# Optimization experiments

Measured on AMD Instinct MI355X. Metric: run time of the kernel, lower is better.

## Reference

```python
import math
import jax, jax.numpy as jnp
import numpy as np

N = 2048
HID = 1024
ALPHA = 0.5
BETA = 0.1  # greedy term is zero when coords is None


def setup_inputs() -> dict:
    key = jax.random.key(0)
    k1, k2, k3, k4 = jax.random.split(key, 4)
    node_emb = jax.random.normal(k1, (N, HID), jnp.float32)
    demands = jax.random.uniform(k2, (N,), jnp.float32)  # each < 1 << capacity
    # query_net: Linear(hid+2 -> hid); key_net: Linear(hid -> hid)
    Wq = jax.random.normal(k3, (HID, HID + 2), jnp.float32) / math.sqrt(HID + 2)
    bq = jnp.zeros((HID,), jnp.float32)
    Wk = jax.random.normal(k4, (HID, HID), jnp.float32) / math.sqrt(HID)
    bk = jnp.zeros((HID,), jnp.float32)
    return {"node_emb": node_emb, "demands": demands, "Wq": Wq, "bq": bq,
            "Wk": Wk, "bk": bk, "capacity": 40, "depot_idx": 0}


def _decode(node_emb, demands, Wq, bq, Wk, bk, capacity, depot_idx):
    n, h = node_emb.shape
    cap = jnp.float32(capacity)
    inv_sqrt = 1.0 / math.sqrt(h)
    # key_net is a per-node linear map: precompute once (same math as per-step gather+linear)
    K = node_emb @ Wk.T + bk  # [N, H]
    idx = jnp.arange(n)
    # demands < 1, capacity = 40 => >= 39 customers per route => few depot returns;
    # T = N + N//8 safely bounds customer picks + route-closing depot emissions.
    T = n + n // 8
    visited0 = jnp.zeros((n,), bool).at[depot_idx].set(True)

    def step(carry, _):
        visited, load, last, done = carry
        feasible = (~visited) & (demands <= load)
        has_cand = jnp.any(feasible)
        # context = [emb(last), load/capacity, avgd]; avgd = 0 since coords is None
        ctx = jnp.concatenate([node_emb[last],
                               jnp.stack([load / cap, jnp.float32(0.0)])])
        q = Wq @ ctx + bq                      # [H]
        s = ALPHA * ((K @ q) * inv_sqrt)       # [N] scores over all nodes
        s_m = jnp.where(feasible, s, -jnp.inf)
        cand = jnp.argmax(s_m)
        take = has_cand & (~done)
        nxt = jnp.where(take, cand, depot_idx).astype(jnp.int32)
        step_score = jnp.where(take, s[cand], jnp.float32(0.0))
        visited = visited | ((idx == cand) & take)
        load = jnp.where(take, load - demands[cand], cap)  # route end resets load
        done = done | ((~take) & jnp.all(visited))
        return (visited, load, nxt, done), (nxt, step_score)

    carry0 = (visited0, cap, jnp.int32(depot_idx), jnp.bool_(False))
    _, (seq, scores) = jax.lax.scan(step, carry0, None, length=T)
    tour = jnp.concatenate([jnp.array([depot_idx], seq.dtype), seq])  # [T+1]
    return tour, scores


def reference(node_emb, demands, Wq, bq, Wk, bk, capacity, depot_idx):
    # tour: flat visitation order; routes are the segments between depot occurrences
    # (trailing depots are padding once all customers are served).
    # scores: selected decoder score at each step (0 at depot/padding steps).
    return _decode(node_emb, demands, Wq, bq, Wk, bk, capacity, depot_idx)
```

## Files before the change

kernel.cpp:

```cpp
#include <hip/hip_runtime.h>
#include <hip/hip_bf16.h>


#define NN 2048
#define HH 1024
#define TSTEPS (NN + NN / 8)
#define TILE 64
#define KT 16
#define KCAND 128

__global__ __launch_bounds__(256) void prep_wqh(const float* __restrict__ Wq,
                                                float* __restrict__ Wqh) {
  int id = blockIdx.x * 256 + threadIdx.x;
  int r = id >> 10, c = id & 1023;
  Wqh[id] = Wq[r * (HH + 2) + c];
}

__global__ __launch_bounds__(256) void gemm_nt(const float* __restrict__ A, int lda,
                                               const float* __restrict__ B, int ldb,
                                               float* __restrict__ C, int ldc,
                                               int K, const float* __restrict__ bias) {
  __shared__ float As[KT][TILE + 4];
  __shared__ float Bs[KT][TILE + 4];
  const int i0 = blockIdx.y * TILE;
  const int j0 = blockIdx.x * TILE;
  const int t = threadIdx.x;
  const int srow = t >> 2, sq = t & 3;
  const int tx = t & 15, ty = t >> 4;
  float acc[4][4] = {};
  for (int k0 = 0; k0 < K; k0 += KT) {
    float4 av = *(const float4*)&A[(size_t)(i0 + srow) * lda + k0 + sq * 4];
    float4 bv = *(const float4*)&B[(size_t)(j0 + srow) * ldb + k0 + sq * 4];
    __syncthreads();
    As[sq * 4 + 0][srow] = av.x; As[sq * 4 + 1][srow] = av.y;
    As[sq * 4 + 2][srow] = av.z; As[sq * 4 + 3][srow] = av.w;
    Bs[sq * 4 + 0][srow] = bv.x; Bs[sq * 4 + 1][srow] = bv.y;
    Bs[sq * 4 + 2][srow] = bv.z; Bs[sq * 4 + 3][srow] = bv.w;
    __syncthreads();
#pragma unroll
    for (int k = 0; k < KT; ++k) {
      float4 a4 = *(const float4*)&As[k][ty * 4];
      float4 b4 = *(const float4*)&Bs[k][tx * 4];
      float a[4] = {a4.x, a4.y, a4.z, a4.w};
      float b[4] = {b4.x, b4.y, b4.z, b4.w};
#pragma unroll
      for (int m = 0; m < 4; ++m)
#pragma unroll
        for (int n = 0; n < 4; ++n) acc[m][n] = fmaf(a[m], b[n], acc[m][n]);
    }
  }
  float bb[4] = {0.f, 0.f, 0.f, 0.f};
  if (bias) {
#pragma unroll
    for (int n = 0; n < 4; ++n) bb[n] = bias[j0 + tx * 4 + n];
  }
#pragma unroll
  for (int m = 0; m < 4; ++m) {
    float4 st = {acc[m][0] + bb[0], acc[m][1] + bb[1], acc[m][2] + bb[2], acc[m][3] + bb[3]};
    *(float4*)&C[(size_t)(i0 + ty * 4 + m) * ldc + j0 + tx * 4] = st;
  }
}

__global__ __launch_bounds__(64) void uv_k(const float* __restrict__ Kmat,
                                           const float* __restrict__ Wq,
                                           const float* __restrict__ bq,
                                           float* __restrict__ u, float* __restrict__ v) {
  int i = blockIdx.x;
  int lane = threadIdx.x;
  float su = 0.f, sv = 0.f;
#pragma unroll
  for (int m = 0; m < HH / 64; ++m) {
    int j = lane + 64 * m;
    float kv = Kmat[(size_t)i * HH + j];
    su = fmaf(kv, Wq[(size_t)j * (HH + 2) + HH], su);
    sv = fmaf(kv, bq[j], sv);
  }
#pragma unroll
  for (int off = 32; off; off >>= 1) {
    su += __shfl_down(su, off, 64);
    sv += __shfl_down(sv, off, 64);
  }
  if (lane == 0) { u[i] = su; v[i] = sv; }
}

__global__ __launch_bounds__(256) void umax_k(const float* __restrict__ u,
                                              float* __restrict__ umaxp) {
  __shared__ float sm[256];
  int t = threadIdx.x;
  float m = 0.f;
  for (int i = t; i < NN; i += 256) m = fmaxf(m, fabsf(u[i]));
  sm[t] = m;
  __syncthreads();
  for (int s = 128; s; s >>= 1) {
    if (t < s) sm[t] = fmaxf(sm[t], sm[t + s]);
    __syncthreads();
  }
  if (t == 0) *umaxp = sm[0];
}

__device__ __forceinline__ unsigned f2key(float f) {
  unsigned x = __float_as_uint(f);
  return x ^ ((x >> 31) ? 0xFFFFFFFFu : 0x80000000u);
}
__device__ __forceinline__ float key2f(unsigned k) {
  unsigned x = (k & 0x80000000u) ? (k ^ 0x80000000u) : ~k;
  return __uint_as_float(x);
}
__global__ __launch_bounds__(256) void prep_cand(const float* __restrict__ GT,
                                                 uint2* __restrict__ cand,
                                                 float* __restrict__ thr) {
  __shared__ float rowv[NN];
  __shared__ int hist[256];
  __shared__ int s_d, s_need, s_gt, s_eq;
  const int row = blockIdx.x, t = threadIdx.x;
  for (int i = t; i < NN; i += 256) rowv[i] = GT[(size_t)row * NN + i];
  __syncthreads();
  unsigned prefix = 0;
  int need = KCAND;
  for (int pass = 0; pass < 4; ++pass) {
    hist[t] = 0;
    __syncthreads();
    const int shift = 24 - 8 * pass;
    for (int i = t; i < NN; i += 256) {
      unsigned k = f2key(rowv[i]);
      if (pass == 0 || (k >> (shift + 8)) == (prefix >> (shift + 8)))
        atomicAdd(&hist[(k >> shift) & 0xFF], 1);
    }
    __syncthreads();
    if (t == 0) {
      int cum = 0, d = 255;
      for (; d > 0; --d) {
        if (cum + hist[d] >= need) break;
        cum += hist[d];
      }
      s_d = d;
      s_need = need - cum;
    }
    __syncthreads();
    prefix |= ((unsigned)s_d) << shift;
    need = s_need;
    __syncthreads();
  }
  const unsigned thrk = prefix;
  if (t == 0) { s_gt = 0; s_eq = 0; thr[row] = key2f(thrk); }
  __syncthreads();
  for (int i = t; i < NN; i += 256) {
    if (f2key(rowv[i]) > thrk) {
      int p = atomicAdd(&s_gt, 1);
      cand[(size_t)row * KCAND + p] = make_uint2(__float_as_uint(rowv[i]), (unsigned)i);
    }
  }
  __syncthreads();
  const int cgt = s_gt;
  for (int i = t; i < NN; i += 256) {
    if (f2key(rowv[i]) == thrk) {
      int p = atomicAdd(&s_eq, 1);
      if (p < KCAND - cgt)
        cand[(size_t)row * KCAND + cgt + p] = make_uint2(__float_as_uint(rowv[i]), (unsigned)i);
    }
  }
}

__global__ __launch_bounds__(256) void warm_k(const float* __restrict__ a, int n,
                                              const float* __restrict__ b, int m,
                                              float* __restrict__ sink) {
  float s = 0.f;
  const float4* a4 = (const float4*)a;
  for (int i = threadIdx.x; i < n / 4; i += 256) {
    float4 x = a4[i];
    s += x.x + x.y + x.z + x.w;
  }
  for (int i = threadIdx.x; i < m; i += 256) s += b[i];
  if (s == 1.2345e-30f) sink[blockIdx.x] = s;
}

#define DPP_MERGE2(CTRL)                                                      \
  {                                                                           \
    int ovb = __builtin_amdgcn_update_dpp(                                    \
        (int)0xFF800000, __float_as_int(bv), (CTRL), 0xf, 0xf, false);        \
    int oib = __builtin_amdgcn_update_dpp(                                    \
        0x7fffffff, bi, (CTRL), 0xf, 0xf, false);                             \
    float ov = __int_as_float(ovb);                                           \
    if (ov > bv || (ov == bv && oib < bi)) { bv = ov; bi = oib; }             \
  }

__global__ __launch_bounds__(64, 1) void decode(const float* __restrict__ GT,
                                                const uint2* __restrict__ cand,
                                                const float* __restrict__ thrp,
                                                const float* __restrict__ umaxp,
                                                const float* __restrict__ u,
                                                const float* __restrict__ demands,
                                                const int* __restrict__ capp,
                                                const int* __restrict__ depotp,
                                                float* __restrict__ out) {
  __shared__ __align__(16) float s_dem[NN];
  __shared__ __align__(16) float s_dd[NN];
  __shared__ __align__(16) float s_u[NN];
  __shared__ __align__(16) uint4 s_dcand[KCAND / 2];
  __shared__ __align__(16) float s_tour[TSTEPS + 1];
  __shared__ __align__(16) float s_lr[TSTEPS];

  const int lane = threadIdx.x;
  const int depot = *depotp;
  const float capf = (float)(*capp);
  const float umaxv = *umaxp;
  const float INF = __builtin_inff();
  const float NEGINF = -INF;
  const float C0 = 0.015625f;
  const float MARGIN = 0.5f;

  for (int i = lane; i < NN; i += 64) {
    float d = demands[i];
    s_dem[i] = d;
    s_dd[i] = d;
    s_u[i] = u[i];
  }
  const uint4* dc4 = (const uint4*)(cand + (size_t)depot * KCAND);
  for (int i = lane; i < KCAND / 2; i += 64) s_dcand[i] = dc4[i];
  const float thrd = thrp[depot];
  __syncthreads();
  if (lane == 0) {
    s_dd[depot] = INF;
    s_tour[0] = (float)depot;
  }

  float uu[32];
#pragma unroll
  for (int r = 0; r < 8; ++r) {
    float4 u4 = ((const float4*)u)[r * 64 + lane];
    uu[r * 4 + 0] = u4.x; uu[r * 4 + 1] = u4.y;
    uu[r * 4 + 2] = u4.z; uu[r * 4 + 3] = u4.w;
  }

  const float4* dd4 = (const float4*)s_dd;

  int done = 0, ntaken = 0, lasts = depot;
  float load = capf;
  float lr = load / capf;
  float thrcur = thrd;
  uint4 ca = dc4[lane];

  for (int step = 0; step < TSTEPS; ++step) {
    if (done) {
      const float df = (float)depot;
      for (int q = step + lane; q < TSTEPS; q += 64) {
        s_tour[1 + q] = df;
        s_lr[q] = -1.0f;
      }
      break;
    }
    float bv = NEGINF;
    int bi = 0x7fffffff;
    {
      float g0 = __uint_as_float(ca.x); int i0 = (int)ca.y;
      float g1 = __uint_as_float(ca.z); int i1 = (int)ca.w;
      float d0 = s_dd[i0], u0 = s_u[i0];
      float d1 = s_dd[i1], u1 = s_u[i1];
      float t0 = fmaf(u0, lr, g0);
      float t1 = fmaf(u1, lr, g1);
      if ((d0 <= load) && (t0 > bv || (t0 == bv && i0 < bi))) { bv = t0; bi = i0; }
      if ((d1 <= load) && (t1 > bv || (t1 == bv && i1 < bi))) { bv = t1; bi = i1; }
    }
    DPP_MERGE2(0x111); DPP_MERGE2(0x112); DPP_MERGE2(0x114);
    DPP_MERGE2(0x118); DPP_MERGE2(0x142); DPP_MERGE2(0x143);
    float rbv = __int_as_float(__builtin_amdgcn_readlane(__float_as_int(bv), 63));
    int rbi = __builtin_amdgcn_readlane(bi, 63);

    const float B = fmaf(lr, umaxv, thrcur) + MARGIN;
    int take, nxt;
    if (rbv > B) {
      take = 1; nxt = rbi;
    } else {
      const float4* rowp = (const float4*)(GT + (size_t)lasts * NN);
      float bv = NEGINF;
      int bi = NN;
#pragma unroll
      for (int r = 0; r < 8; ++r) {
        float4 g4 = rowp[r * 64 + lane];
        float4 d4 = dd4[r * 64 + lane];
        float gl[4] = {g4.x, g4.y, g4.z, g4.w};
        float dl[4] = {d4.x, d4.y, d4.z, d4.w};
        float cv = NEGINF;
        int cj = 0;
#pragma unroll
        for (int j = 0; j < 4; ++j) {
          float tt = fmaf(uu[r * 4 + j], lr, gl[j]);
          bool feas = (dl[j] <= load);
          if (feas && tt > cv) { cv = tt; cj = j; }
        }
        if (cv > bv) { bv = cv; bi = 4 * (r * 64 + lane) + cj; }
      }
      DPP_MERGE2(0x111); DPP_MERGE2(0x112); DPP_MERGE2(0x114);
      DPP_MERGE2(0x118); DPP_MERGE2(0x142); DPP_MERGE2(0x143);
      float fbv = __int_as_float(__builtin_amdgcn_readlane(__float_as_int(bv), 63));
      rbi = __builtin_amdgcn_readlane(bi, 63);
      take = (fbv > NEGINF);
      nxt = take ? rbi : depot;
    }

    if (nxt == depot) {
      ca = s_dcand[lane];
      thrcur = thrd;
    } else {
      const uint4* rc4 = (const uint4*)(cand + (size_t)nxt * KCAND);
      ca = rc4[lane];
      thrcur = thrp[nxt];
    }

    if (lane == 0) {
      s_tour[1 + step] = (float)nxt;
      s_lr[step] = take ? lr : -1.0f;
    }
    if (take) {
      load = load - s_dem[rbi];
      ntaken++;
      if (lane == 0) s_dd[rbi] = INF;
    } else {
      load = capf;
      if (ntaken == NN - 1) done = 1;
    }
    lasts = nxt;
    lr = load / capf;
  }

  for (int i = lane; i <= TSTEPS; i += 64) out[i] = s_tour[i];
  for (int s = lane; s < TSTEPS; s += 64) {
    float lrs = s_lr[s];
    float sc = 0.0f;
    if (lrs >= 0.0f) {
      int lastI = (int)s_tour[s];
      int biI = (int)s_tour[s + 1];
      float g = GT[(size_t)lastI * NN + biI];
      sc = fmaf(u[biI], lrs, g) * C0;
    }
    out[1 + TSTEPS + s] = sc;
  }
}

extern "C" void kernel_launch(void* const* d_in, const int* in_sizes, int n_in,
                              void* d_out, int out_size, void* d_ws, size_t ws_size,
                              hipStream_t stream) {
  const float* emb     = (const float*)d_in[0];
  const float* demands = (const float*)d_in[1];
  const float* Wq      = (const float*)d_in[2];
  const float* bq      = (const float*)d_in[3];
  const float* Wk      = (const float*)d_in[4];
  const float* bk      = (const float*)d_in[5];
  const int* cap       = (const int*)d_in[6];
  const int* depot     = (const int*)d_in[7];
  float* out           = (float*)d_out;

  char* ws = (char*)d_ws;
  float* Kmat = (float*)(ws);
  float* Z    = (float*)(ws + ((size_t)8 << 20));
  float* GT   = (float*)(ws + ((size_t)16 << 20));
  float* Wqh  = (float*)(ws + ((size_t)32 << 20));
  float* u    = (float*)(ws + ((size_t)36 << 20));
  float* v    = (float*)(ws + ((size_t)36 << 20) + 8192);
  float* thr  = (float*)(ws + ((size_t)36 << 20) + 16384);
  float* umax = (float*)(ws + ((size_t)36 << 20) + 24576);
  float* sink = (float*)(ws + ((size_t)36 << 20) + 32768);
  uint2* cnd  = (uint2*)Wqh;

  hipLaunchKernelGGL(prep_wqh, dim3(4096), dim3(256), 0, stream, Wq, Wqh);
  hipLaunchKernelGGL(gemm_nt, dim3(HH / TILE, NN / TILE), dim3(256), 0, stream,
                     emb, HH, Wk, HH, Kmat, HH, HH, bk);
  hipLaunchKernelGGL(gemm_nt, dim3(HH / TILE, NN / TILE), dim3(256), 0, stream,
                     emb, HH, Wqh, HH, Z, HH, HH, (const float*)nullptr);
  hipLaunchKernelGGL(uv_k, dim3(NN), dim3(64), 0, stream, Kmat, Wq, bq, u, v);
  hipLaunchKernelGGL(umax_k, dim3(1), dim3(256), 0, stream, u, umax);
  hipLaunchKernelGGL(gemm_nt, dim3(NN / TILE, NN / TILE), dim3(256), 0, stream,
                     Z, HH, Kmat, HH, GT, NN, HH, v);
  hipLaunchKernelGGL(prep_cand, dim3(NN), dim3(256), 0, stream, GT, cnd, thr);
  hipLaunchKernelGGL(warm_k, dim3(128), dim3(256), 0, stream,
                     (const float*)cnd, NN * KCAND * 2, thr, NN, sink);
  hipLaunchKernelGGL(decode, dim3(1), dim3(64), 0, stream, GT, cnd, thr, umax,
                     u, demands, cap, depot, out);
}
```

Before: 2.043 ms.

## Add compact top-15 packed candidate tier in LDS before 128-candidate fallback

prep_cand now also picks the top-15 candidates per row and packs each into one 32-bit word holding a truncated score key and an 11-bit index. It also writes a per-row threshold, set to infinity when scores are too large for the truncation to be safe. The decode kernel copies all packed lists into LDS and checks this first tier with a top-2 DPP reduction plus margin tests. It falls back to the 128-candidate global list and then to a full row scan only when needed. The step loop is unrolled by three with software-prefetched candidate loads, trading a large LDS footprint and extra prep work for shorter serial per-step latency.

Measured after the change: 2.202 ms. 7.8% more time.

```diff
diff --git a/kernel.cpp b/kernel.cpp
--- a/kernel.cpp
+++ b/kernel.cpp
@@ -8,6 +8,7 @@
 #define TILE 64
 #define KT 16
 #define KCAND 128
+#define KL 15
 
 __global__ __launch_bounds__(256) void prep_wqh(const float* __restrict__ Wq,
                                                 float* __restrict__ Wqh) {
@@ -108,10 +109,14 @@
 }
 __global__ __launch_bounds__(256) void prep_cand(const float* __restrict__ GT,
                                                  uint2* __restrict__ cand,
-                                                 float* __restrict__ thr) {
+                                                 float* __restrict__ thr,
+                                                 unsigned* __restrict__ pc16,
+                                                 float* __restrict__ thr16) {
   __shared__ float rowv[NN];
   __shared__ int hist[256];
-  __shared__ int s_d, s_need, s_gt, s_eq;
+  __shared__ unsigned c128k[KCAND];
+  __shared__ int c128i[KCAND];
+  __shared__ int s_d, s_need, s_gt, s_eq, s_gt2, s_eq2, s_flag;
   const int row = blockIdx.x, t = threadIdx.x;
   for (int i = t; i < NN; i += 256) rowv[i] = GT[(size_t)row * NN + i];
   __syncthreads();
@@ -145,9 +150,12 @@
   if (t == 0) { s_gt = 0; s_eq = 0; thr[row] = key2f(thrk); }
   __syncthreads();
   for (int i = t; i < NN; i += 256) {
-    if (f2key(rowv[i]) > thrk) {
+    unsigned k = f2key(rowv[i]);
+    if (k > thrk) {
       int p = atomicAdd(&s_gt, 1);
       cand[(size_t)row * KCAND + p] = make_uint2(__float_as_uint(rowv[i]), (unsigned)i);
+      c128k[p] = k;
+      c128i[p] = i;
     }
   }
   __syncthreads();
@@ -155,10 +163,62 @@
   for (int i = t; i < NN; i += 256) {
     if (f2key(rowv[i]) == thrk) {
       int p = atomicAdd(&s_eq, 1);
-      if (p < KCAND - cgt)
+      if (p < KCAND - cgt) {
         cand[(size_t)row * KCAND + cgt + p] = make_uint2(__float_as_uint(rowv[i]), (unsigned)i);
-    }
-  }
+        c128k[cgt + p] = thrk;
+        c128i[cgt + p] = i;
+      }
+    }
+  }
+  __syncthreads();
+  unsigned pfx2 = 0;
+  need = KL;
+  for (int pass = 0; pass < 4; ++pass) {
+    hist[t] = 0;
+    __syncthreads();
+    const int shift = 24 - 8 * pass;
+    for (int i = t; i < KCAND; i += 256) {
+      unsigned k = c128k[i];
+      if (pass == 0 || (k >> (shift + 8)) == (pfx2 >> (shift + 8)))
+        atomicAdd(&hist[(k >> shift) & 0xFF], 1);
+    }
+    __syncthreads();
+    if (t == 0) {
+      int cum = 0, d = 255;
+      for (; d > 0; --d) {
+        if (cum + hist[d] >= need) break;
+        cum += hist[d];
+      }
+      s_d = d;
+      s_need = need - cum;
+    }
+    __syncthreads();
+    pfx2 |= ((unsigned)s_d) << shift;
+    need = s_need;
+    __syncthreads();
+  }
+  const unsigned thrk15 = pfx2;
+  if (t == 0) { s_gt2 = 0; s_eq2 = 0; s_flag = 0; }
+  __syncthreads();
+  for (int i = t; i < KCAND; i += 256) {
+    if (c128k[i] > thrk15) {
+      int p = atomicAdd(&s_gt2, 1);
+      pc16[(size_t)row * KL + p] = (c128k[i] & 0xFFFFF800u) | (unsigned)c128i[i];
+      if (fabsf(key2f(c128k[i])) >= 128.0f) s_flag = 1;
+    }
+  }
+  __syncthreads();
+  const int cgt2 = s_gt2;
+  for (int i = t; i < KCAND; i += 256) {
+    if (c128k[i] == thrk15) {
+      int p = atomicAdd(&s_eq2, 1);
+      if (p < KL - cgt2)
+        pc16[(size_t)row * KL + cgt2 + p] = (thrk15 & 0xFFFFF800u) | (unsigned)c128i[i];
+    }
+  }
+  if (t == 0 && fabsf(key2f(thrk15)) >= 128.0f) s_flag = 1;
+  __syncthreads();
+  if (t == 0) thr16[row] = s_flag ? __builtin_inff() : key2f(thrk15);
 }
 
 __global__ __launch_bounds__(256) void warm_k(const float* __restrict__ a, int n,
@@ -184,21 +244,38 @@
     if (ov > bv || (ov == bv && oib < bi)) { bv = ov; bi = oib; }             \
   }
 
+#define DPP_TOP2(CTRL)                                                        \
+  {                                                                           \
+    int ovb = __builtin_amdgcn_update_dpp(                                    \
+        (int)0xFF800000, __float_as_int(bv1), (CTRL), 0xf, 0xf, false);       \
+    int oib = __builtin_amdgcn_update_dpp(                                    \
+        0x7fffffff, bi1, (CTRL), 0xf, 0xf, false);                            \
+    int ov2b = __builtin_amdgcn_update_dpp(                                   \
+        (int)0xFF800000, __float_as_int(bv2), (CTRL), 0xf, 0xf, false);       \
+    float ov1 = __int_as_float(ovb);                                          \
+    float ov2 = __int_as_float(ov2b);                                         \
+    float lose = fminf(bv1, ov1);                                             \
+    if (ov1 > bv1 || (ov1 == bv1 && oib < bi1)) { bv1 = ov1; bi1 = oib; }     \
+    bv2 = fmaxf(fmaxf(bv2, ov2), lose);                                       \
+  }
+
 __global__ __launch_bounds__(64, 1) void decode(const float* __restrict__ GT,
                                                 const uint2* __restrict__ cand,
                                                 const float* __restrict__ thrp,
+                                                const unsigned* __restrict__ pc16,
+                                                const float* __restrict__ thr16,
                                                 const float* __restrict__ umaxp,
                                                 const float* __restrict__ u,
                                                 const float* __restrict__ demands,
                                                 const int* __restrict__ capp,
                                                 const int* __restrict__ depotp,
                                                 float* __restrict__ out) {
-  __shared__ __align__(16) float s_dem[NN];
+  __shared__ __align__(16) unsigned s_pc[NN * KL + 64];
   __shared__ __align__(16) float s_dd[NN];
   __shared__ __align__(16) float s_u[NN];
-  __shared__ __align__(16) uint4 s_dcand[KCAND / 2];
-  __shared__ __align__(16) float s_tour[TSTEPS + 1];
+  __shared__ __align__(16) float s_thr[NN];
   __shared__ __align__(16) float s_lr[TSTEPS];
+  __shared__ __align__(16) unsigned short s_tour[TSTEPS + 2];
 
   const int lane = threadIdx.x;
   const int depot = *depotp;
@@ -208,122 +285,143 @@
   const float NEGINF = -INF;
   const float C0 = 0.015625f;
   const float MARGIN = 0.5f;
+  const float EGM = 0.0625f;
 
   for (int i = lane; i < NN; i += 64) {
-    float d = demands[i];
-    s_dem[i] = d;
-    s_dd[i] = d;
+    s_dd[i] = demands[i];
     s_u[i] = u[i];
-  }
-  const uint4* dc4 = (const uint4*)(cand + (size_t)depot * KCAND);
-  for (int i = lane; i < KCAND / 2; i += 64) s_dcand[i] = dc4[i];
-  const float thrd = thrp[depot];
-  __syncthreads();
+    s_thr[i] = thr16[i];
+  }
+  {
+    const uint4* p4 = (const uint4*)pc16;
+    uint4* q4 = (uint4*)s_pc;
+    for (int i = lane; i < NN * KL / 4; i += 64) q4[i] = p4[i];
+  }
   if (lane == 0) {
     s_dd[depot] = INF;
-    s_tour[0] = (float)depot;
-  }
-
-  float uu[32];
-#pragma unroll
-  for (int r = 0; r < 8; ++r) {
-    float4 u4 = ((const float4*)u)[r * 64 + lane];
-    uu[r * 4 + 0] = u4.x; uu[r * 4 + 1] = u4.y;
-    uu[r * 4 + 2] = u4.z; uu[r * 4 + 3] = u4.w;
-  }
-
-  const float4* dd4 = (const float4*)s_dd;
+    s_tour[0] = (unsigned short)depot;
+  }
 
   int done = 0, ntaken = 0, lasts = depot;
   float load = capf;
   float lr = load / capf;
-  float thrcur = thrd;
-  uint4 ca = dc4[lane];
-
-  for (int step = 0; step < TSTEPS; ++step) {
-    if (done) {
-      const float df = (float)depot;
-      for (int q = step + lane; q < TSTEPS; q += 64) {
-        s_tour[1 + q] = df;
-        s_lr[q] = -1.0f;
-      }
-      break;
-    }
-    float bv = NEGINF;
-    int bi = 0x7fffffff;
-    {
-      float g0 = __uint_as_float(ca.x); int i0 = (int)ca.y;
-      float g1 = __uint_as_float(ca.z); int i1 = (int)ca.w;
-      float d0 = s_dd[i0], u0 = s_u[i0];
-      float d1 = s_dd[i1], u1 = s_u[i1];
-      float t0 = fmaf(u0, lr, g0);
-      float t1 = fmaf(u1, lr, g1);
-      if ((d0 <= load) && (t0 > bv || (t0 == bv && i0 < bi))) { bv = t0; bi = i0; }
-      if ((d1 <= load) && (t1 > bv || (t1 == bv && i1 < bi))) { bv = t1; bi = i1; }
-    }
-    DPP_MERGE2(0x111); DPP_MERGE2(0x112); DPP_MERGE2(0x114);
-    DPP_MERGE2(0x118); DPP_MERGE2(0x142); DPP_MERGE2(0x143);
-    float rbv = __int_as_float(__builtin_amdgcn_readlane(__float_as_int(bv), 63));
-    int rbi = __builtin_amdgcn_readlane(bi, 63);
-
-    const float B = fmaf(lr, umaxv, thrcur) + MARGIN;
-    int take, nxt;
-    if (rbv > B) {
-      take = 1; nxt = rbi;
-    } else {
-      const float4* rowp = (const float4*)(GT + (size_t)lasts * NN);
-      float bv = NEGINF;
-      int bi = NN;
-#pragma unroll
-      for (int r = 0; r < 8; ++r) {
-        float4 g4 = rowp[r * 64 + lane];
-        float4 d4 = dd4[r * 64 + lane];
-        float gl[4] = {g4.x, g4.y, g4.z, g4.w};
-        float dl[4] = {d4.x, d4.y, d4.z, d4.w};
-        float cv = NEGINF;
-        int cj = 0;
-#pragma unroll
-        for (int j = 0; j < 4; ++j) {
-          float tt = fmaf(uu[r * 4 + j], lr, gl[j]);
-          bool feas = (dl[j] <= load);
-          if (feas && tt > cv) { cv = tt; cj = j; }
-        }
-        if (cv > bv) { bv = cv; bi = 4 * (r * 64 + lane) + cj; }
-      }
-      DPP_MERGE2(0x111); DPP_MERGE2(0x112); DPP_MERGE2(0x114);
-      DPP_MERGE2(0x118); DPP_MERGE2(0x142); DPP_MERGE2(0x143);
-      float fbv = __int_as_float(__builtin_amdgcn_readlane(__float_as_int(bv), 63));
-      rbi = __builtin_amdgcn_readlane(bi, 63);
-      take = (fbv > NEGINF);
-      nxt = take ? rbi : depot;
-    }
-
-    if (nxt == depot) {
-      ca = s_dcand[lane];
-      thrcur = thrd;
-    } else {
-      const uint4* rc4 = (const uint4*)(cand + (size_t)nxt * KCAND);
-      ca = rc4[lane];
-      thrcur = thrp[nxt];
-    }
-
-    if (lane == 0) {
-      s_tour[1 + step] = (float)nxt;
-      s_lr[step] = take ? lr : -1.0f;
-    }
-    if (take) {
-      load = load - s_dem[rbi];
-      ntaken++;
-      if (lane == 0) s_dd[rbi] = INF;
-    } else {
-      load = capf;
-      if (ntaken == NN - 1) done = 1;
-    }
-    lasts = nxt;
-    lr = load / capf;
-  }
-
-  for (int i = lane; i <= TSTEPS; i += 64) out[i] = s_tour[i];
+  int step = 0;
+  uint4 cc0, cc1, cc2;
+  float th0, th1, th2;
+
+#define STEP_ONE(CC, TH)                                                        \
+  {                                                                             \
+    if (done) goto FLUSH;                                                       \
+    const int row = lasts;                                                      \
+                          \
+    CC = ((const uint4*)(cand + (size_t)row * KCAND))[lane];                    \
+    TH = thrp[row];                                                             \
+                                \
+    unsigned pw = s_pc[row * KL + lane];                                        \
+    float thr1 = s_thr[row];                                                    \
+    int i1x = (int)(pw & 0x7FFu);                                               \
+    float g1 = key2f(pw & 0xFFFFF800u);         \
+    float d1 = s_dd[i1x];                                                       \
+    float su1 = s_u[i1x];                                                       \
+    float t1 = fmaf(su1, lr, g1);                                               \
+    bool act = (lane < KL) && (d1 <= load);                                     \
+    float bv1 = act ? t1 : NEGINF;                                              \
+    int bi1 = act ? i1x : 0x7fffffff;                                           \
+    float bv2 = NEGINF;                                                         \
+    DPP_TOP2(0x111); DPP_TOP2(0x112); DPP_TOP2(0x114);                          \
+    DPP_TOP2(0x118); DPP_TOP2(0x142); DPP_TOP2(0x143);                          \
+    float rv1 = __int_as_float(__builtin_amdgcn_readlane(__float_as_int(bv1), 63)); \
+    int ri1 = __builtin_amdgcn_readlane(bi1, 63);                               \
+    float rv2 = __int_as_float(__builtin_amdgcn_readlane(__float_as_int(bv2), 63)); \
+    const float B1 = fmaf(lr, umaxv, thr1) + MARGIN;                            \
+    int take, nxt;                                                              \
+    if (rv1 > B1 && rv1 > rv2 + EGM) {                                          \
+            \
+      take = 1; nxt = ri1;                                                      \
+    } else {                                                                    \
+           \
+      float bv = NEGINF;                                                        \
+      int bi = 0x7fffffff;                                                      \
+      {                                                                         \
+        float ga = __uint_as_float(CC.x); int ia = (int)CC.y;                   \
+        float gb = __uint_as_float(CC.z); int ib = (int)CC.w;                   \
+        float da = s_dd[ia], ua = s_u[ia];                                      \
+        float db = s_dd[ib], ub = s_u[ib];                                      \
+        float ta = fmaf(ua, lr, ga);                                            \
+        float tb = fmaf(ub, lr, gb);                                            \
+        if ((da <= load) && (ta > bv || (ta == bv && ia < bi))) { bv = ta; bi = ia; } \
+        if ((db <= load) && (tb > bv || (tb == bv && ib < bi))) { bv = tb; bi = ib; } \
+      }                                                                         \
+      DPP_MERGE2(0x111); DPP_MERGE2(0x112); DPP_MERGE2(0x114);                  \
+      DPP_MERGE2(0x118); DPP_MERGE2(0x142); DPP_MERGE2(0x143);                  \
+      float rbv = __int_as_float(__builtin_amdgcn_readlane(__float_as_int(bv), 63)); \
+      int rbi = __builtin_amdgcn_readlane(bi, 63);                              \
+      const float B2 = fmaf(lr, umaxv, TH) + MARGIN;                            \
+      if (rbv > B2) {                                                           \
+        take = 1; nxt = rbi;                                                    \
+      } else {                                                                  \
+                              \
+        const float4* rowp = (const float4*)(GT + (size_t)row * NN);            \
+        const float4* dd4 = (const float4*)s_dd;                                \
+        const float4* uu4 = (const float4*)s_u;                                 \
+        float fv = NEGINF;                                                      \
+        int fi = NN;                                                            \
+        _Pragma("unroll") for (int r = 0; r < 8; ++r) {                         \
+          float4 g4 = rowp[r * 64 + lane];                                      \
+          float4 d4v = dd4[r * 64 + lane];                                      \
+          float4 u4v = uu4[r * 64 + lane];                                      \
+          float gl[4] = {g4.x, g4.y, g4.z, g4.w};                               \
+          float dl[4] = {d4v.x, d4v.y, d4v.z, d4v.w};                           \
+          float ul[4] = {u4v.x, u4v.y, u4v.z, u4v.w};                           \
+          float cv = NEGINF;                                                    \
+          int cj = 0;                                                           \
+          _Pragma("unroll") for (int j = 0; j < 4; ++j) {                       \
+            float tt = fmaf(ul[j], lr, gl[j]);                                  \
+            bool feas = (dl[j] <= load);                                        \
+            if (feas && tt > cv) { cv = tt; cj = j; }                           \
+          }                                                                     \
+          if (cv > fv) { fv = cv; fi = 4 * (r * 64 + lane) + cj; }              \
+        }                                                                       \
+        float bv = fv;                                                          \
+        int bi = fi;                                                            \
+        DPP_MERGE2(0x111); DPP_MERGE2(0x112); DPP_MERGE2(0x114);                \
+        DPP_MERGE2(0x118); DPP_MERGE2(0x142); DPP_MERGE2(0x143);                \
+        float fbv = __int_as_float(__builtin_amdgcn_readlane(__float_as_int(bv), 63)); \
+        int fbi = __builtin_amdgcn_readlane(bi, 63);                            \
+        take = (fbv > NEGINF) ? 1 : 0;                                          \
+        nxt = take ? fbi : depot;                                               \
+      }                                                                         \
+    }                                                                           \
+        \
+    if (lane == 0) {                                                            \
+      s_tour[1 + step] = (unsigned short)nxt;                                   \
+      s_lr[step] = take ? lr : -1.0f;                                           \
+    }                                                                           \
+    if (take) {                                                                 \
+      float dwin = s_dd[nxt];          \
+      load = load - dwin;                                                       \
+      ntaken++;                                                                 \
+      if (lane == 0) s_dd[nxt] = INF;                                           \
+    } else {                                                                    \
+      load = capf;                                                              \
+      if (ntaken == NN - 1) done = 1;                                           \
+    }                                                                           \
+    lasts = nxt;                                                                \
+    lr = load / capf;                                                           \
+    ++step;                                                                     \
+  }
+
+  for (int s3 = 0; s3 < TSTEPS; s3 += 3) {
+    STEP_ONE(cc0, th0)
+    STEP_ONE(cc1, th1)
+    STEP_ONE(cc2, th2)
+  }
+FLUSH:
+  for (int q = step + lane; q < TSTEPS; q += 64) {
+    s_tour[1 + q] = (unsigned short)depot;
+    s_lr[q] = -1.0f;
+  }
+  for (int i = lane; i <= TSTEPS; i += 64) out[i] = (float)s_tour[i];
   for (int s = lane; s < TSTEPS; s += 64) {
     float lrs = s_lr[s];
     float sc = 0.0f;
@@ -331,10 +429,11 @@
       int lastI = (int)s_tour[s];
       int biI = (int)s_tour[s + 1];
       float g = GT[(size_t)lastI * NN + biI];
-      sc = fmaf(u[biI], lrs, g) * C0;
+      sc = fmaf(s_u[biI], lrs, g) * C0;
     }
     out[1 + TSTEPS + s] = sc;
   }
+#undef STEP_ONE
 }
 
 extern "C" void kernel_launch(void* const* d_in, const int* in_sizes, int n_in,
@@ -361,6 +460,8 @@
   float* umax = (float*)(ws + ((size_t)36 << 20) + 24576);
   float* sink = (float*)(ws + ((size_t)36 << 20) + 32768);
   uint2* cnd  = (uint2*)Wqh;
+  unsigned* pc16g = (unsigned*)(ws + ((size_t)34 << 20));
+  float* thr16g   = (float*)(ws + ((size_t)34 << 20) + (128 << 10));
 
   hipLaunchKernelGGL(prep_wqh, dim3(4096), dim3(256), 0, stream, Wq, Wqh);
   hipLaunchKernelGGL(gemm_nt, dim3(HH / TILE, NN / TILE), dim3(256), 0, stream,
@@ -371,9 +472,10 @@
   hipLaunchKernelGGL(umax_k, dim3(1), dim3(256), 0, stream, u, umax);
   hipLaunchKernelGGL(gemm_nt, dim3(NN / TILE, NN / TILE), dim3(256), 0, stream,
                      Z, HH, Kmat, HH, GT, NN, HH, v);
-  hipLaunchKernelGGL(prep_cand, dim3(NN), dim3(256), 0, stream, GT, cnd, thr);
+  hipLaunchKernelGGL(prep_cand, dim3(NN), dim3(256), 0, stream, GT, cnd, thr,
+                     pc16g, thr16g);
   hipLaunchKernelGGL(warm_k, dim3(128), dim3(256), 0, stream,
                      (const float*)cnd, NN * KCAND * 2, thr, NN, sink);
-  hipLaunchKernelGGL(decode, dim3(1), dim3(64), 0, stream, GT, cnd, thr, umax,
-                     u, demands, cap, depot, out);
-}
+  hipLaunchKernelGGL(decode, dim3(1), dim3(64), 0, stream, GT, cnd, thr,
+                     pc16g, thr16g, umax, u, demands, cap, depot, out);
+}
```

## Add packed top-15 candidate tier in LDS ahead of top-128 fallback

Applied to the files above, without the earlier changes.

Prep now also extracts each row's top-15 candidates, packed as truncated score bits plus an 11-bit index, and stores two bf16-rounded thresholds per row. The decode kernel keeps the whole top-15 table in LDS and picks from it using a top-2 DPP reduction with a gap check. It falls back to the global top-128 list and then to the full GT row only when that pick is not certifiably correct. This removes most per-step global memory loads from the serial decode loop, but costs a heavier prep pass, about 120KB of LDS, and relies on quantised scores being exact enough to keep argmax results correct.

New measurement: 1.905 ms. -6.8%, faster.

```diff
diff --git a/kernel.cpp b/kernel.cpp
--- a/kernel.cpp
+++ b/kernel.cpp
@@ -8,6 +8,7 @@
 #define TILE 64
 #define KT 16
 #define KCAND 128
+#define KL 15
 
 __global__ __launch_bounds__(256) void prep_wqh(const float* __restrict__ Wq,
                                                 float* __restrict__ Wqh) {
@@ -106,12 +107,20 @@
   unsigned x = (k & 0x80000000u) ? (k ^ 0x80000000u) : ~k;
   return __uint_as_float(x);
 }
+__device__ __forceinline__ unsigned ub16(float x) {
+  unsigned b = __float_as_uint(x);
+  if (x > 0.f && (b & 0xFFFFu)) b += 0x10000u;
+  return b >> 16;
+}
 __global__ __launch_bounds__(256) void prep_cand(const float* __restrict__ GT,
                                                  uint2* __restrict__ cand,
-                                                 float* __restrict__ thr) {
+                                                 unsigned* __restrict__ pc16,
+                                                 unsigned* __restrict__ thrpk) {
   __shared__ float rowv[NN];
   __shared__ int hist[256];
-  __shared__ int s_d, s_need, s_gt, s_eq;
+  __shared__ unsigned c128k[KCAND];
+  __shared__ int c128i[KCAND];
+  __shared__ int s_d, s_need, s_gt, s_eq, s_gt2, s_eq2, s_flag;
   const int row = blockIdx.x, t = threadIdx.x;
   for (int i = t; i < NN; i += 256) rowv[i] = GT[(size_t)row * NN + i];
   __syncthreads();
@@ -142,12 +151,15 @@
     __syncthreads();
   }
   const unsigned thrk = prefix;
-  if (t == 0) { s_gt = 0; s_eq = 0; thr[row] = key2f(thrk); }
+  if (t == 0) { s_gt = 0; s_eq = 0; }
   __syncthreads();
   for (int i = t; i < NN; i += 256) {
-    if (f2key(rowv[i]) > thrk) {
+    unsigned k = f2key(rowv[i]);
+    if (k > thrk) {
       int p = atomicAdd(&s_gt, 1);
       cand[(size_t)row * KCAND + p] = make_uint2(__float_as_uint(rowv[i]), (unsigned)i);
+      c128k[p] = k;
+      c128i[p] = i;
     }
   }
   __syncthreads();
@@ -155,14 +167,68 @@
   for (int i = t; i < NN; i += 256) {
     if (f2key(rowv[i]) == thrk) {
       int p = atomicAdd(&s_eq, 1);
-      if (p < KCAND - cgt)
+      if (p < KCAND - cgt) {
         cand[(size_t)row * KCAND + cgt + p] = make_uint2(__float_as_uint(rowv[i]), (unsigned)i);
-    }
+        c128k[cgt + p] = thrk;
+        c128i[cgt + p] = i;
+      }
+    }
+  }
+  __syncthreads();
+  unsigned pfx2 = 0;
+  need = KL;
+  for (int pass = 0; pass < 4; ++pass) {
+    hist[t] = 0;
+    __syncthreads();
+    const int shift = 24 - 8 * pass;
+    for (int i = t; i < KCAND; i += 256) {
+      unsigned k = c128k[i];
+      if (pass == 0 || (k >> (shift + 8)) == (pfx2 >> (shift + 8)))
+        atomicAdd(&hist[(k >> shift) & 0xFF], 1);
+    }
+    __syncthreads();
+    if (t == 0) {
+      int cum = 0, d = 255;
+      for (; d > 0; --d) {
+        if (cum + hist[d] >= need) break;
+        cum += hist[d];
+      }
+      s_d = d;
+      s_need = need - cum;
+    }
+    __syncthreads();
+    pfx2 |= ((unsigned)s_d) << shift;
+    need = s_need;
+    __syncthreads();
+  }
+  const unsigned thrk15 = pfx2;
+  if (t == 0) { s_gt2 = 0; s_eq2 = 0; s_flag = 0; }
+  __syncthreads();
+  for (int i = t; i < KCAND; i += 256) {
+    if (c128k[i] > thrk15) {
+      int p = atomicAdd(&s_gt2, 1);
+      pc16[(size_t)row * KL + p] = (c128k[i] & 0xFFFFF800u) | (unsigned)c128i[i];
+      if (fabsf(key2f(c128k[i])) >= 128.0f) s_flag = 1;
+    }
+  }
+  __syncthreads();
+  const int cgt2 = s_gt2;
+  for (int i = t; i < KCAND; i += 256) {
+    if (c128k[i] == thrk15) {
+      int p = atomicAdd(&s_eq2, 1);
+      if (p < KL - cgt2)
+        pc16[(size_t)row * KL + cgt2 + p] = (thrk15 & 0xFFFFF800u) | (unsigned)c128i[i];
+    }
+  }
+  if (t == 0 && fabsf(key2f(thrk15)) >= 128.0f) s_flag = 1;
+  __syncthreads();
+  if (t == 0) {
+    float t15 = s_flag ? __builtin_inff() : key2f(thrk15);
+    thrpk[row] = (ub16(t15) << 16) | ub16(key2f(thrk));
   }
 }
 
 __global__ __launch_bounds__(256) void warm_k(const float* __restrict__ a, int n,
-                                              const float* __restrict__ b, int m,
                                               float* __restrict__ sink) {
   float s = 0.f;
   const float4* a4 = (const float4*)a;
@@ -170,7 +236,6 @@
     float4 x = a4[i];
     s += x.x + x.y + x.z + x.w;
   }
-  for (int i = threadIdx.x; i < m; i += 256) s += b[i];
   if (s == 1.2345e-30f) sink[blockIdx.x] = s;
 }
 
@@ -184,21 +249,36 @@
     if (ov > bv || (ov == bv && oib < bi)) { bv = ov; bi = oib; }             \
   }
 
+#define DPP_TOP2(CTRL)                                                        \
+  {                                                                           \
+    int ovb = __builtin_amdgcn_update_dpp(                                    \
+        (int)0xFF800000, __float_as_int(bv1), (CTRL), 0xf, 0xf, false);       \
+    int oib = __builtin_amdgcn_update_dpp(                                    \
+        0x7fffffff, bi1, (CTRL), 0xf, 0xf, false);                            \
+    int ov2b = __builtin_amdgcn_update_dpp(                                   \
+        (int)0xFF800000, __float_as_int(bv2), (CTRL), 0xf, 0xf, false);       \
+    float ov1 = __int_as_float(ovb);                                          \
+    float ov2 = __int_as_float(ov2b);                                         \
+    float lose = fminf(bv1, ov1);                                             \
+    if (ov1 > bv1 || (ov1 == bv1 && oib < bi1)) { bv1 = ov1; bi1 = oib; }     \
+    bv2 = fmaxf(fmaxf(bv2, ov2), lose);                                       \
+  }
+
 __global__ __launch_bounds__(64, 1) void decode(const float* __restrict__ GT,
                                                 const uint2* __restrict__ cand,
-                                                const float* __restrict__ thrp,
+                                                const unsigned* __restrict__ pc16,
+                                                const unsigned* __restrict__ thrpkg,
                                                 const float* __restrict__ umaxp,
                                                 const float* __restrict__ u,
                                                 const float* __restrict__ demands,
                                                 const int* __restrict__ capp,
                                                 const int* __restrict__ depotp,
                                                 float* __restrict__ out) {
-  __shared__ __align__(16) float s_dem[NN];
-  __shared__ __align__(16) float s_dd[NN];
-  __shared__ __align__(16) float s_u[NN];
-  __shared__ __align__(16) uint4 s_dcand[KCAND / 2];
-  __shared__ __align__(16) float s_tour[TSTEPS + 1];
+  __shared__ __align__(16) unsigned s_pc[NN * KL + 64];
+  __shared__ __align__(16) float2 s_du[NN];
+  __shared__ __align__(16) unsigned s_thr[NN];
   __shared__ __align__(16) float s_lr[TSTEPS];
+  __shared__ __align__(16) unsigned short s_tour[TSTEPS + 2];
 
   const int lane = threadIdx.x;
   const int depot = *depotp;
@@ -208,122 +288,129 @@
   const float NEGINF = -INF;
   const float C0 = 0.015625f;
   const float MARGIN = 0.5f;
+  const float EGM = 0.0625f;
+  float* sduf = (float*)s_du;
 
   for (int i = lane; i < NN; i += 64) {
-    float d = demands[i];
-    s_dem[i] = d;
-    s_dd[i] = d;
-    s_u[i] = u[i];
-  }
-  const uint4* dc4 = (const uint4*)(cand + (size_t)depot * KCAND);
-  for (int i = lane; i < KCAND / 2; i += 64) s_dcand[i] = dc4[i];
-  const float thrd = thrp[depot];
-  __syncthreads();
+    s_du[i] = make_float2(demands[i], u[i]);
+    s_thr[i] = thrpkg[i];
+  }
+  {
+    const uint4* p4 = (const uint4*)pc16;
+    uint4* q4 = (uint4*)s_pc;
+    for (int i = lane; i < NN * KL / 4; i += 64) q4[i] = p4[i];
+  }
   if (lane == 0) {
-    s_dd[depot] = INF;
-    s_tour[0] = (float)depot;
-  }
-
-  float uu[32];
-#pragma unroll
-  for (int r = 0; r < 8; ++r) {
-    float4 u4 = ((const float4*)u)[r * 64 + lane];
-    uu[r * 4 + 0] = u4.x; uu[r * 4 + 1] = u4.y;
-    uu[r * 4 + 2] = u4.z; uu[r * 4 + 3] = u4.w;
-  }
-
-  const float4* dd4 = (const float4*)s_dd;
+    sduf[2 * depot] = INF;
+    s_tour[0] = (unsigned short)depot;
+  }
 
   int done = 0, ntaken = 0, lasts = depot;
   float load = capf;
   float lr = load / capf;
-  float thrcur = thrd;
-  uint4 ca = dc4[lane];
-
-  for (int step = 0; step < TSTEPS; ++step) {
-    if (done) {
-      const float df = (float)depot;
-      for (int q = step + lane; q < TSTEPS; q += 64) {
-        s_tour[1 + q] = df;
-        s_lr[q] = -1.0f;
-      }
-      break;
-    }
-    float bv = NEGINF;
-    int bi = 0x7fffffff;
-    {
-      float g0 = __uint_as_float(ca.x); int i0 = (int)ca.y;
-      float g1 = __uint_as_float(ca.z); int i1 = (int)ca.w;
-      float d0 = s_dd[i0], u0 = s_u[i0];
-      float d1 = s_dd[i1], u1 = s_u[i1];
-      float t0 = fmaf(u0, lr, g0);
-      float t1 = fmaf(u1, lr, g1);
-      if ((d0 <= load) && (t0 > bv || (t0 == bv && i0 < bi))) { bv = t0; bi = i0; }
-      if ((d1 <= load) && (t1 > bv || (t1 == bv && i1 < bi))) { bv = t1; bi = i1; }
-    }
-    DPP_MERGE2(0x111); DPP_MERGE2(0x112); DPP_MERGE2(0x114);
-    DPP_MERGE2(0x118); DPP_MERGE2(0x142); DPP_MERGE2(0x143);
-    float rbv = __int_as_float(__builtin_amdgcn_readlane(__float_as_int(bv), 63));
-    int rbi = __builtin_amdgcn_readlane(bi, 63);
-
-    const float B = fmaf(lr, umaxv, thrcur) + MARGIN;
+  int step = 0;
+  const int lcl = (lane < KL) ? lane : (KL - 1);
+
+  for (; step < TSTEPS; ++step) {
+    const int row = lasts;
+    unsigned pw = s_pc[row * KL + lcl];
+    unsigned pk = s_thr[row];
+    int i1x = (int)(pw & 0x7FFu);
+    float g1 = key2f(pw & 0xFFFFF800u);
+    float2 du1 = s_du[i1x];
+    float t1 = fmaf(du1.y, lr, g1);
+    bool act = (lane < KL) && (du1.x <= load);
+    float bv1 = act ? t1 : NEGINF;
+    int bi1 = act ? i1x : 0x7fffffff;
+    float bv2 = NEGINF;
+    DPP_TOP2(0x111); DPP_TOP2(0x112); DPP_TOP2(0x114); DPP_TOP2(0x118);
+    float rv1 = __int_as_float(__builtin_amdgcn_readlane(__float_as_int(bv1), 15));
+    int ri1 = __builtin_amdgcn_readlane(bi1, 15);
+    float rv2 = __int_as_float(__builtin_amdgcn_readlane(__float_as_int(bv2), 15));
+    float thr1 = __uint_as_float(pk & 0xFFFF0000u);
+    const float B1 = fmaf(lr, umaxv, thr1) + MARGIN;
     int take, nxt;
-    if (rbv > B) {
-      take = 1; nxt = rbi;
+    if (rv1 > B1 && rv1 > rv2 + EGM) {
+      take = 1; nxt = ri1;
     } else {
-      const float4* rowp = (const float4*)(GT + (size_t)lasts * NN);
+      uint4 cc = ((const uint4*)(cand + (size_t)row * KCAND))[lane];
       float bv = NEGINF;
-      int bi = NN;
-#pragma unroll
-      for (int r = 0; r < 8; ++r) {
-        float4 g4 = rowp[r * 64 + lane];
-        float4 d4 = dd4[r * 64 + lane];
-        float gl[4] = {g4.x, g4.y, g4.z, g4.w};
-        float dl[4] = {d4.x, d4.y, d4.z, d4.w};
-        float cv = NEGINF;
-        int cj = 0;
-#pragma unroll
-        for (int j = 0; j < 4; ++j) {
-          float tt = fmaf(uu[r * 4 + j], lr, gl[j]);
-          bool feas = (dl[j] <= load);
-          if (feas && tt > cv) { cv = tt; cj = j; }
-        }
-        if (cv > bv) { bv = cv; bi = 4 * (r * 64 + lane) + cj; }
+      int bi = 0x7fffffff;
+      {
+        float ga = __uint_as_float(cc.x); int ia = (int)cc.y;
+        float gb = __uint_as_float(cc.z); int ib = (int)cc.w;
+        float2 da = s_du[ia];
+        float2 db = s_du[ib];
+        float ta = fmaf(da.y, lr, ga);
+        float tb = fmaf(db.y, lr, gb);
+        if ((da.x <= load) && (ta > bv || (ta == bv && ia < bi))) { bv = ta; bi = ia; }
+        if ((db.x <= load) && (tb > bv || (tb == bv && ib < bi))) { bv = tb; bi = ib; }
       }
       DPP_MERGE2(0x111); DPP_MERGE2(0x112); DPP_MERGE2(0x114);
       DPP_MERGE2(0x118); DPP_MERGE2(0x142); DPP_MERGE2(0x143);
-      float fbv = __int_as_float(__builtin_amdgcn_readlane(__float_as_int(bv), 63));
-      rbi = __builtin_amdgcn_readlane(bi, 63);
-      take = (fbv > NEGINF);
-      nxt = take ? rbi : depot;
-    }
-
-    if (nxt == depot) {
-      ca = s_dcand[lane];
-      thrcur = thrd;
-    } else {
-      const uint4* rc4 = (const uint4*)(cand + (size_t)nxt * KCAND);
-      ca = rc4[lane];
-      thrcur = thrp[nxt];
+      float rbv = __int_as_float(__builtin_amdgcn_readlane(__float_as_int(bv), 63));
+      int rbi = __builtin_amdgcn_readlane(bi, 63);
+      float thr2 = __uint_as_float(pk << 16);
+      const float B2 = fmaf(lr, umaxv, thr2) + MARGIN;
+      if (rbv > B2) {
+        take = 1; nxt = rbi;
+      } else {
+        const float4* rowp = (const float4*)(GT + (size_t)row * NN);
+        const float4* du4 = (const float4*)s_du;
+        float fv = NEGINF;
+        int fi = NN;
+#pragma unroll
+        for (int r = 0; r < 8; ++r) {
+          float4 g4 = rowp[r * 64 + lane];
+          float4 pA = du4[(r * 64 + lane) * 2];
+          float4 pB = du4[(r * 64 + lane) * 2 + 1];
+          float gl[4] = {g4.x, g4.y, g4.z, g4.w};
+          float dl[4] = {pA.x, pA.z, pB.x, pB.z};
+          float ul[4] = {pA.y, pA.w, pB.y, pB.w};
+          float cv = NEGINF;
+          int cj = 0;
+#pragma unroll
+          for (int j = 0; j < 4; ++j) {
+            float tt = fmaf(ul[j], lr, gl[j]);
+            bool feas = (dl[j] <= load);
+            if (feas && tt > cv) { cv = tt; cj = j; }
+          }
+          if (cv > fv) { fv = cv; fi = 4 * (r * 64 + lane) + cj; }
+        }
+        float bv = fv;
+        int bi = fi;
+        DPP_MERGE2(0x111); DPP_MERGE2(0x112); DPP_MERGE2(0x114);
+        DPP_MERGE2(0x118); DPP_MERGE2(0x142); DPP_MERGE2(0x143);
+        float fbv = __int_as_float(__builtin_amdgcn_readlane(__float_as_int(bv), 63));
+        int fbi = __builtin_amdgcn_readlane(bi, 63);
+        take = (fbv > NEGINF) ? 1 : 0;
+        nxt = take ? fbi : depot;
+      }
     }
 
     if (lane == 0) {
-      s_tour[1 + step] = (float)nxt;
+      s_tour[1 + step] = (unsigned short)nxt;
       s_lr[step] = take ? lr : -1.0f;
     }
     if (take) {
-      load = load - s_dem[rbi];
+      float dwin = s_du[nxt].x;
+      load = load - dwin;
       ntaken++;
-      if (lane == 0) s_dd[rbi] = INF;
+      if (lane == 0) sduf[2 * nxt] = INF;
     } else {
       load = capf;
       if (ntaken == NN - 1) done = 1;
     }
     lasts = nxt;
     lr = load / capf;
-  }
-
-  for (int i = lane; i <= TSTEPS; i += 64) out[i] = s_tour[i];
+    if (done) { ++step; break; }
+  }
+
+  for (int q = step + lane; q < TSTEPS; q += 64) {
+    s_tour[1 + q] = (unsigned short)depot;
+    s_lr[q] = -1.0f;
+  }
+  for (int i = lane; i <= TSTEPS; i += 64) out[i] = (float)s_tour[i];
   for (int s = lane; s < TSTEPS; s += 64) {
     float lrs = s_lr[s];
     float sc = 0.0f;
@@ -331,7 +418,7 @@
       int lastI = (int)s_tour[s];
       int biI = (int)s_tour[s + 1];
       float g = GT[(size_t)lastI * NN + biI];
-      sc = fmaf(u[biI], lrs, g) * C0;
+      sc = fmaf(s_du[biI].y, lrs, g) * C0;
     }
     out[1 + TSTEPS + s] = sc;
   }
@@ -357,10 +444,11 @@
   float* Wqh  = (float*)(ws + ((size_t)32 << 20));
   float* u    = (float*)(ws + ((size_t)36 << 20));
   float* v    = (float*)(ws + ((size_t)36 << 20) + 8192);
-  float* thr  = (float*)(ws + ((size_t)36 << 20) + 16384);
+  unsigned* thrpkg = (unsigned*)(ws + ((size_t)36 << 20) + 16384);
   float* umax = (float*)(ws + ((size_t)36 << 20) + 24576);
   float* sink = (float*)(ws + ((size_t)36 << 20) + 32768);
   uint2* cnd  = (uint2*)Wqh;
+  unsigned* pc16g = (unsigned*)(ws + ((size_t)34 << 20));
 
   hipLaunchKernelGGL(prep_wqh, dim3(4096), dim3(256), 0, stream, Wq, Wqh);
   hipLaunchKernelGGL(gemm_nt, dim3(HH / TILE, NN / TILE), dim3(256), 0, stream,
@@ -371,9 +459,10 @@
   hipLaunchKernelGGL(umax_k, dim3(1), dim3(256), 0, stream, u, umax);
   hipLaunchKernelGGL(gemm_nt, dim3(NN / TILE, NN / TILE), dim3(256), 0, stream,
                      Z, HH, Kmat, HH, GT, NN, HH, v);
-  hipLaunchKernelGGL(prep_cand, dim3(NN), dim3(256), 0, stream, GT, cnd, thr);
+  hipLaunchKernelGGL(prep_cand, dim3(NN), dim3(256), 0, stream, GT, cnd,
+                     pc16g, thrpkg);
   hipLaunchKernelGGL(warm_k, dim3(128), dim3(256), 0, stream,
-                     (const float*)cnd, NN * KCAND * 2, thr, NN, sink);
-  hipLaunchKernelGGL(decode, dim3(1), dim3(64), 0, stream, GT, cnd, thr, umax,
-                     u, demands, cap, depot, out);
-}
+                     (const float*)cnd, NN * KCAND * 2, sink);
+  hipLaunchKernelGGL(decode, dim3(1), dim3(64), 0, stream, GT, cnd,
+                     pc16g, thrpkg, umax, u, demands, cap, depot, out);
+}
```
